# Kernel tuning notes

Measured on AMD Instinct MI355X. Metric: run time of the kernel, lower is better.

The kernel has to match this reference:

```python
import jax, jax.numpy as jnp
import numpy as np

NUM_NODES = 5000
NUM_RELS = 100
MAX_VISIT = 20
EMB = 128
HID = 128
OUT = 25
LAYERS = 3
B = 32
N_TOTAL = 100000
E_TOTAL = 400000
DECAY_RATE = 0.01
EPS = 0.0  # GIN-style self-loop weight (self_attn=0.0, not trained)


def setup_inputs() -> dict:
    key = jax.random.key(0)
    ks = jax.random.split(key, 24)
    f32 = jnp.float32
    # graph structure
    node_ids = jax.random.randint(ks[0], (N_TOTAL,), 0, NUM_NODES)
    rel_ids = jax.random.randint(ks[1], (E_TOTAL,), 0, NUM_RELS)
    edge_index = jax.random.randint(ks[2], (2, E_TOTAL), 0, N_TOTAL)
    batch = jnp.sort(jax.random.randint(ks[3], (N_TOTAL,), 0, B))
    # binary visit/ehr indicators (float, fed into Linear layers / masks)
    visit_node = (jax.random.uniform(ks[4], (B, MAX_VISIT, NUM_NODES)) < 0.05).astype(f32)
    ehr_nodes = (jax.random.uniform(ks[5], (B, NUM_NODES)) < 0.2).astype(f32)
    # embedding tables + projection
    node_table = jax.random.normal(ks[6], (NUM_NODES, EMB), f32) * 0.02
    rel_table = jax.random.normal(ks[7], (NUM_RELS, EMB), f32) * 0.02
    lin_w = jax.random.normal(ks[8], (HID, EMB), f32) * (1.0 / np.sqrt(EMB))
    lin_b = jnp.zeros((HID,), f32)
    # per-layer params, stacked on leading axis
    alpha_w = jax.random.normal(ks[9], (LAYERS, NUM_NODES, NUM_NODES), f32) * np.sqrt(1.0 / NUM_NODES)
    alpha_b = jnp.zeros((LAYERS, NUM_NODES), f32)
    beta_w = jax.random.normal(ks[10], (LAYERS, 1, NUM_NODES), f32) * np.sqrt(2.0 / (NUM_NODES + 1))
    beta_b = jnp.zeros((LAYERS, 1), f32)
    wr_w = jax.random.normal(ks[11], (LAYERS, 1, HID), f32) * (1.0 / np.sqrt(HID))
    wr_b = jnp.zeros((LAYERS, 1), f32)
    conv_w = jax.random.normal(ks[12], (LAYERS, HID, HID), f32) * (1.0 / np.sqrt(HID))
    conv_b = jnp.zeros((LAYERS, HID), f32)
    # final MLP (joint mode: Linear(2H,H) -> ReLU -> Linear(H,OUT))
    mlp_w1 = jax.random.normal(ks[13], (HID, 2 * HID), f32) * (1.0 / np.sqrt(2 * HID))
    mlp_b1 = jnp.zeros((HID,), f32)
    mlp_w2 = jax.random.normal(ks[14], (OUT, HID), f32) * (1.0 / np.sqrt(HID))
    mlp_b2 = jnp.zeros((OUT,), f32)
    return dict(node_table=node_table, rel_table=rel_table, lin_w=lin_w, lin_b=lin_b,
                alpha_w=alpha_w, alpha_b=alpha_b, beta_w=beta_w, beta_b=beta_b,
                wr_w=wr_w, wr_b=wr_b, conv_w=conv_w, conv_b=conv_b,
                mlp_w1=mlp_w1, mlp_b1=mlp_b1, mlp_w2=mlp_w2, mlp_b2=mlp_b2,
                visit_node=visit_node, ehr_nodes=ehr_nodes,
                node_ids=node_ids, rel_ids=rel_ids, edge_index=edge_index, batch=batch)


def reference(node_table, rel_table, lin_w, lin_b, alpha_w, alpha_b, beta_w, beta_b,
              wr_w, wr_b, conv_w, conv_b, mlp_w1, mlp_b1, mlp_w2, mlp_b2,
              visit_node, ehr_nodes, node_ids, rel_ids, edge_index, batch):
    # embed + project (lin is shared by nodes and relations)
    x = node_table[node_ids] @ lin_w.T + lin_b        # [N, H]
    e = rel_table[rel_ids] @ lin_w.T + lin_b          # [E, H]
    src, dst = edge_index[0], edge_index[1]
    N = x.shape[0]
    # temporal decay lambda_j = exp(gamma * (V - j)), shape [1, V, 1]
    j = jnp.arange(MAX_VISIT, dtype=x.dtype)
    lam = jnp.exp(DECAY_RATE * (MAX_VISIT - j))[None, :, None]
    for l in range(LAYERS):
        # alpha: softmax over visit dim of Linear(num_nodes -> num_nodes)
        alpha = jax.nn.softmax(jnp.einsum('bvn,mn->bvm', visit_node, alpha_w[l]) + alpha_b[l], axis=1)  # [B,V,num_nodes]
        # beta: tanh(Linear(num_nodes -> 1)) * lambda_j
        beta = jnp.tanh(jnp.einsum('bvn,on->bvo', visit_node, beta_w[l]) + beta_b[l]) * lam  # [B,V,1]
        attn = jnp.sum(alpha * beta, axis=1)          # [B, num_nodes]
        # per-edge attention gathered at the source node j of each edge
        attn_e = attn[batch[src], node_ids[src]][:, None]   # [E,1]
        # BAT message: relu(x_j * attn_j + W_R(e) * e), scatter-add at dst
        w_rel = e @ wr_w[l].T + wr_b[l]               # [E,1]
        msg = jax.nn.relu(x[src] * attn_e + w_rel * e)
        agg = jax.ops.segment_sum(msg, dst, num_segments=N)
        x = (agg + (1.0 + EPS) * x) @ conv_w[l].T + conv_b[l]
    # patient_mode='joint': global mean pool + masked EHR-node mean
    cnt = jax.ops.segment_sum(jnp.ones((N,), x.dtype), batch, num_segments=B)
    x_graph = jax.ops.segment_sum(x, batch, num_segments=B) / jnp.maximum(cnt, 1.0)[:, None]
    mask = ehr_nodes[batch, node_ids]                 # [N], 0/1
    mcnt = jax.ops.segment_sum(mask, batch, num_segments=B)
    x_node = jax.ops.segment_sum(x * mask[:, None], batch, num_segments=B) / jnp.maximum(mcnt, 1.0)[:, None]
    h = jnp.concatenate([x_graph, x_node], axis=1)    # [B, 2H]
    h = jax.nn.relu(h @ mlp_w1.T + mlp_b1)
    return h @ mlp_w2.T + mlp_b2                      # [B, OUT] logits


if __name__ == '__main__':
    out = reference(**setup_inputs())
    print(out.shape)
```

## Files before the change

### kernel.cpp

```cpp
#include <hip/hip_runtime.h>
#include <stdint.h>

#define NNODE 5000
#define NREL  100
#define MAXV  20
#define NH    128
#define NBATCH 32
#define NTOT  100000
#define ETOT  400000
#define AKP   5056

typedef float  f32x4  __attribute__((ext_vector_type(4)));
typedef __bf16 bf16x8 __attribute__((ext_vector_type(8)));

static __device__ __forceinline__ f32x4 f4zero(){ f32x4 z; z[0]=0.f; z[1]=0.f; z[2]=0.f; z[3]=0.f; return z; }
static __device__ __forceinline__ int swz(int row, int byte_in_row){ return byte_in_row ^ ((row & 7) << 4); }

__global__ __launch_bounds__(256) void gemm128f(
    const float* __restrict__ A0, const float* __restrict__ A1, int boundary, int M,
    const float* __restrict__ W, const float* __restrict__ bias,
    float* __restrict__ D0, float* __restrict__ D1)
{
  __shared__ __bf16 As[64*128];
  __shared__ __bf16 Bh[128*128];
  __shared__ __bf16 Bl[128*128];
  char* AsB = (char*)As; char* BhB = (char*)Bh; char* BlB = (char*)Bl;
  const int tid = threadIdx.x, lane = tid & 63, w = tid >> 6;
  const int r0 = blockIdx.x * 64;
  {
    const int row = tid >> 2, c0 = (tid & 3) * 32;
    const int gr = r0 + row;
    bf16x8 t8[4];
    if (gr < M){
      const float* src = (gr < boundary) ? (A0 + (size_t)gr * NH) : (A1 + (size_t)(gr - boundary) * NH);
      const f32x4* gp = (const f32x4*)(src + c0);
      #pragma unroll
      for (int j = 0; j < 8; ++j){
        f32x4 v = gp[j];
        #pragma unroll
        for (int q = 0; q < 4; ++q) t8[j>>1][(j&1)*4+q] = (__bf16)v[q];
      }
    } else {
      #pragma unroll
      for (int j = 0; j < 4; ++j)
        #pragma unroll
        for (int q = 0; q < 8; ++q) t8[j][q] = (__bf16)0.0f;
    }
    #pragma unroll
    for (int j = 0; j < 4; ++j) *(bf16x8*)(AsB + swz(row, row*256 + c0*2 + j*16) ) = t8[j];
  }
  {
    const int row = tid >> 1, c0 = (tid & 1) * 64;
    bf16x8 th[8], tl[8];
    const f32x4* gp = (const f32x4*)(W + row*NH + c0);
    #pragma unroll
    for (int j = 0; j < 16; ++j){
      f32x4 v = gp[j];
      #pragma unroll
      for (int q = 0; q < 4; ++q){
        float f = v[q];
        __bf16 h = (__bf16)f;
        th[j>>1][(j&1)*4+q] = h;
        tl[j>>1][(j&1)*4+q] = (__bf16)(f - (float)h);
      }
    }
    #pragma unroll
    for (int j = 0; j < 8; ++j){
      *(bf16x8*)(BhB + swz(row, row*256 + c0*2 + j*16)) = th[j];
      *(bf16x8*)(BlB + swz(row, row*256 + c0*2 + j*16)) = tl[j];
    }
  }
  __syncthreads();
  f32x4 acc[8];
  #pragma unroll
  for (int n = 0; n < 8; ++n) acc[n] = f4zero();
  #pragma unroll
  for (int kk = 0; kk < 4; ++kk){
    const int kb = kk*64 + (lane>>4)*16;
    const int arow = w*16 + (lane&15);
    bf16x8 af = *(const bf16x8*)(AsB + swz(arow, arow*256 + kb));
    #pragma unroll
    for (int nj = 0; nj < 8; ++nj){
      const int brow = nj*16 + (lane&15);
      bf16x8 bh = *(const bf16x8*)(BhB + swz(brow, brow*256 + kb));
      acc[nj] = __builtin_amdgcn_mfma_f32_16x16x32_bf16(af, bh, acc[nj], 0, 0, 0);
      bf16x8 bl = *(const bf16x8*)(BlB + swz(brow, brow*256 + kb));
      acc[nj] = __builtin_amdgcn_mfma_f32_16x16x32_bf16(af, bl, acc[nj], 0, 0, 0);
    }
  }
  const int rb = r0 + w*16 + ((lane>>4)*4);
  #pragma unroll
  for (int q = 0; q < 4; ++q){
    const int row = rb + q;
    if (row < M){
      #pragma unroll
      for (int nj = 0; nj < 8; ++nj){
        const int col = nj*16 + (lane&15);
        float* dp = (row < boundary) ? (D0 + (size_t)row*NH + col) : (D1 + (size_t)(row-boundary)*NH + col);
        *dp = acc[nj][q] + bias[col];
      }
    }
  }
}

__global__ __launch_bounds__(256) void alpha_gemm(
    const float* __restrict__ W, const __bf16* __restrict__ VNb, float* __restrict__ S)
{
  __shared__ __bf16 As[64*64];
  __shared__ __bf16 Bs[64*64];
  char* AsB = (char*)As; char* BsB = (char*)Bs;
  const int tid = threadIdx.x, lane = tid & 63, w = tid >> 6;
  const int bid = blockIdx.x;
  const int xcd = bid & 7, idx = bid >> 3;
  const int logical = (xcd < 6 ? xcd*99 : 6*99 + (xcd-6)*98) + idx;
  const int mt = logical / 10, bt = logical % 10;

  const int srow = tid >> 2, sc = tid & 3;
  const int gm = mt*64 + srow;
  const bool m_ok = (gm < NNODE);
  const float* wrow = W + (size_t)gm * NNODE;
  const __bf16* vrow = VNb + (size_t)(bt*64 + srow) * AKP;

  f32x4 acc[4];
  #pragma unroll
  for (int n = 0; n < 4; ++n) acc[n] = f4zero();

  bf16x8 avr[2];
  f32x4  bvr[4];
  #pragma unroll
  for (int h = 0; h < 2; ++h) avr[h] = *(const bf16x8*)(vrow + sc*16 + h*8);
  if (m_ok){
    const f32x4* gp = (const f32x4*)(wrow + sc*16);
    #pragma unroll
    for (int j = 0; j < 4; ++j) bvr[j] = gp[j];
  } else {
    #pragma unroll
    for (int j = 0; j < 4; ++j) bvr[j] = f4zero();
  }

  for (int kt = 0; kt < 79; ++kt){
    __syncthreads();
    #pragma unroll
    for (int h = 0; h < 2; ++h)
      *(bf16x8*)(AsB + swz(srow, srow*128 + sc*32 + h*16)) = avr[h];
    {
      bf16x8 t8[2];
      #pragma unroll
      for (int j = 0; j < 4; ++j)
        #pragma unroll
        for (int q = 0; q < 4; ++q) t8[j>>1][(j&1)*4+q] = (__bf16)bvr[j][q];
      #pragma unroll
      for (int h = 0; h < 2; ++h)
        *(bf16x8*)(BsB + swz(srow, srow*128 + sc*32 + h*16)) = t8[h];
    }
    __syncthreads();
    if (kt < 78){
      const int k0 = (kt+1)*64;
      #pragma unroll
      for (int h = 0; h < 2; ++h) avr[h] = *(const bf16x8*)(vrow + k0 + sc*16 + h*8);
      if (!m_ok){
        #pragma unroll
        for (int j = 0; j < 4; ++j) bvr[j] = f4zero();
      } else if (kt + 1 < 78){
        const f32x4* gp = (const f32x4*)(wrow + k0 + sc*16);
        #pragma unroll
        for (int j = 0; j < 4; ++j) bvr[j] = gp[j];
      } else {
        #pragma unroll
        for (int j = 0; j < 4; ++j){
          f32x4 v;
          #pragma unroll
          for (int q = 0; q < 4; ++q){
            int c = k0 + sc*16 + j*4 + q;
            v[q] = (c < NNODE) ? wrow[c] : 0.f;
          }
          bvr[j] = v;
        }
      }
    }
    #pragma unroll
    for (int kk = 0; kk < 2; ++kk){
      const int kb = kk*64 + (lane>>4)*16;
      const int arow = w*16 + (lane&15);
      bf16x8 af = *(const bf16x8*)(AsB + swz(arow, arow*128 + kb));
      #pragma unroll
      for (int nj = 0; nj < 4; ++nj){
        const int brow = nj*16 + (lane&15);
        bf16x8 bf = *(const bf16x8*)(BsB + swz(brow, brow*128 + kb));
        acc[nj] = __builtin_amdgcn_mfma_f32_16x16x32_bf16(af, bf, acc[nj], 0, 0, 0);
      }
    }
  }
  const int rb = bt*64 + w*16 + ((lane>>4)*4);
  #pragma unroll
  for (int nj = 0; nj < 4; ++nj){
    const int col = mt*64 + nj*16 + (lane&15);
    if (col < NNODE){
      #pragma unroll
      for (int q = 0; q < 4; ++q)
        S[(size_t)(rb + q)*NNODE + col] = acc[nj][q];
    }
  }
}

__global__ __launch_bounds__(256) void vn_kernel(const float* __restrict__ visit, __bf16* __restrict__ VNb){
  int id = blockIdx.x*256 + threadIdx.x;
  if (id >= 640*632) return;
  int r = id / 632, c8 = (id % 632) * 8;
  bf16x8 o;
  #pragma unroll
  for (int j = 0; j < 8; ++j){
    int c = c8 + j;
    float v = (c < NNODE) ? visit[(size_t)r*NNODE + c] : 0.f;
    o[j] = (__bf16)v;
  }
  *(bf16x8*)(VNb + (size_t)r*AKP + c8) = o;
}

__global__ __launch_bounds__(256) void x_init_kernel(const float* __restrict__ nproj, const int* __restrict__ nids, float* __restrict__ x){
  int id = blockIdx.x*256 + threadIdx.x;
  int r = id >> 7, f = id & 127;
  x[id] = nproj[(size_t)nids[r]*NH + f];
}

__global__ __launch_bounds__(256) void edge_pre_kernel(const int* __restrict__ esrc, const int* __restrict__ batch, const int* __restrict__ nids, int* __restrict__ eix){
  int e = blockIdx.x*256 + threadIdx.x;
  if (e >= ETOT) return;
  int s = esrc[e];
  eix[e] = batch[s]*NNODE + nids[s];
}

__global__ __launch_bounds__(256) void hist_kernel(const int* __restrict__ edst, int* __restrict__ cnt){
  int e = blockIdx.x*256 + threadIdx.x;
  if (e >= ETOT) return;
  atomicAdd(&cnt[edst[e]], 1);
}

__global__ __launch_bounds__(256) void scan1_kernel(const int* __restrict__ cnt, int* __restrict__ offp, int* __restrict__ bsum){
  __shared__ int sh[256];
  int t = threadIdx.x;
  int base = blockIdx.x*1024 + t*4;
  int v[4]; int ts = 0;
  #pragma unroll
  for (int i = 0; i < 4; ++i){ v[i] = (base+i < NTOT) ? cnt[base+i] : 0; ts += v[i]; }
  sh[t] = ts; __syncthreads();
  for (int o = 1; o < 256; o <<= 1){
    int xv = 0; if (t >= o) xv = sh[t-o];
    __syncthreads();
    if (t >= o) sh[t] += xv;
    __syncthreads();
  }
  int run = sh[t] - ts;
  #pragma unroll
  for (int i = 0; i < 4; ++i){ if (base+i < NTOT) offp[base+i] = run; run += v[i]; }
  if (t == 255) bsum[blockIdx.x] = sh[255];
}

__global__ __launch_bounds__(128) void scan2_kernel(const int* __restrict__ bsum, int* __restrict__ bpre){
  __shared__ int sh[128];
  int t = threadIdx.x;
  int v = (t < 98) ? bsum[t] : 0;
  sh[t] = v; __syncthreads();
  for (int o = 1; o < 128; o <<= 1){
    int xv = 0; if (t >= o) xv = sh[t-o];
    __syncthreads();
    if (t >= o) sh[t] += xv;
    __syncthreads();
  }
  if (t < 98) bpre[t] = sh[t] - v;
}

__global__ __launch_bounds__(256) void scan3_kernel(const int* __restrict__ bpre, int* __restrict__ offp, int* __restrict__ curp){
  int i = blockIdx.x*256 + threadIdx.x;
  if (i >= NTOT) return;
  int v = offp[i] + bpre[i >> 10];
  offp[i] = v; curp[i] = v;
}

__global__ __launch_bounds__(256) void scatter_kernel(const int* __restrict__ edst, int* __restrict__ curp, int* __restrict__ perm){
  int e = blockIdx.x*256 + threadIdx.x;
  if (e >= ETOT) return;
  int p = atomicAdd(&curp[edst[e]], 1);
  perm[p] = e;
}

__global__ __launch_bounds__(256) void beta_kernel(const float* __restrict__ visit, const float* __restrict__ bw, const float* __restrict__ bb, float* __restrict__ beta){
  int wid = blockIdx.x*4 + (threadIdx.x >> 6);
  int lane = threadIdx.x & 63;
  if (wid >= 3*640) return;
  int l = wid / 640, r = wid % 640, vv = r % MAXV;
  const float* vp = visit + (size_t)r*NNODE;
  const float* wp = bw + (size_t)l*NNODE;
  float acc = 0.f;
  for (int n = lane; n < NNODE; n += 64) acc += vp[n]*wp[n];
  #pragma unroll
  for (int o = 32; o > 0; o >>= 1) acc += __shfl_down(acc, o);
  if (lane == 0) beta[wid] = tanhf(acc + bb[l]) * expf(0.01f*(float)(MAXV - vv));
}

__global__ __launch_bounds__(320) void wrel_kernel(const float* __restrict__ relp, const float* __restrict__ wrw, const float* __restrict__ wrb, float* __restrict__ wrel){
  int t = threadIdx.x;
  if (t >= 300) return;
  int l = t / 100, r = t % 100;
  float acc = 0.f;
  for (int h = 0; h < NH; ++h) acc += relp[r*NH + h]*wrw[l*NH + h];
  wrel[t] = acc + wrb[l];
}

__global__ __launch_bounds__(256) void attn_kernel(const float* __restrict__ S, const float* __restrict__ beta_l, float* __restrict__ attn){
  int id = blockIdx.x*256 + threadIdx.x;
  if (id >= NBATCH*NNODE) return;
  int b = id / NNODE;
  const float* sp = S + (size_t)(b*MAXV)*NNODE + (id % NNODE);
  float mx = -1e30f;
  #pragma unroll
  for (int v = 0; v < MAXV; ++v) mx = fmaxf(mx, sp[(size_t)v*NNODE]);
  float den = 0.f, num = 0.f;
  #pragma unroll
  for (int v = 0; v < MAXV; ++v){
    float e = expf(sp[(size_t)v*NNODE] - mx);
    den += e; num += e * beta_l[b*MAXV + v];
  }
  attn[id] = num / den;
}

__global__ __launch_bounds__(256) void agg_kernel(
    const float* __restrict__ x, const float* __restrict__ attn,
    const float* __restrict__ relp, const float* __restrict__ wrel_l,
    const int* __restrict__ eix, const int* __restrict__ esrc, const int* __restrict__ erel,
    const int* __restrict__ offp, const int* __restrict__ cnt, const int* __restrict__ perm,
    float* __restrict__ y)
{
  int node = blockIdx.x*4 + (threadIdx.x >> 6);
  int lane = threadIdx.x & 63;
  float a1 = x[(size_t)node*NH + lane];
  float a2 = x[(size_t)node*NH + 64 + lane];
  int st = offp[node], n = cnt[node];
  for (int t = 0; t < n; ++t){
    int eid = perm[st + t];
    int s  = esrc[eid];
    int rr = erel[eid];
    float at = attn[eix[eid]];
    float wv = wrel_l[rr];
    float x1 = x[(size_t)s*NH + lane];
    float x2 = x[(size_t)s*NH + 64 + lane];
    float r1 = relp[rr*NH + lane];
    float r2 = relp[rr*NH + 64 + lane];
    a1 += fmaxf(x1*at + wv*r1, 0.f);
    a2 += fmaxf(x2*at + wv*r2, 0.f);
  }
  y[(size_t)node*NH + lane] = a1;
  y[(size_t)node*NH + 64 + lane] = a2;
}

__global__ __launch_bounds__(128) void pool_kernel(
    const float* __restrict__ x, const int* __restrict__ batch, const int* __restrict__ nids, const float* __restrict__ ehr,
    float* __restrict__ sum_g, float* __restrict__ sum_n, float* __restrict__ cntb, float* __restrict__ mcntb)
{
  int t = threadIdx.x;
  int r0 = blockIdx.x*128;
  int rend = (r0 + 128 < NTOT) ? r0 + 128 : NTOT;
  float ag = 0.f, an = 0.f, c = 0.f, mc = 0.f; int cur = -1;
  for (int r = r0; r < rend; ++r){
    int b = batch[r];
    if (b != cur){
      if (cur >= 0){
        atomicAdd(&sum_g[cur*NH + t], ag);
        atomicAdd(&sum_n[cur*NH + t], an);
        if (t == 0){ atomicAdd(&cntb[cur], c); atomicAdd(&mcntb[cur], mc); }
      }
      cur = b; ag = an = c = mc = 0.f;
    }
    float xv = x[(size_t)r*NH + t];
    float m = ehr[b*NNODE + nids[r]];
    ag += xv; an += m*xv; c += 1.f; mc += m;
  }
  if (cur >= 0){
    atomicAdd(&sum_g[cur*NH + t], ag);
    atomicAdd(&sum_n[cur*NH + t], an);
    if (t == 0){ atomicAdd(&cntb[cur], c); atomicAdd(&mcntb[cur], mc); }
  }
}

__global__ __launch_bounds__(256) void mlp_kernel(
    const float* __restrict__ sum_g, const float* __restrict__ sum_n, const float* __restrict__ cntb, const float* __restrict__ mcntb,
    const float* __restrict__ w1, const float* __restrict__ b1, const float* __restrict__ w2, const float* __restrict__ b2,
    float* __restrict__ out)
{
  __shared__ float hs[8*256];
  __shared__ float w1s[64*132];
  __shared__ float hid[8*128];
  int t = threadIdx.x;
  int b0 = blockIdx.x * 8;
  for (int e = t; e < 8*256; e += 256){
    int bb = e >> 8, c = e & 255;
    int gb = b0 + bb;
    float v;
    if (c < NH) v = sum_g[gb*NH + c] / fmaxf(cntb[gb], 1.f);
    else        v = sum_n[gb*NH + (c-NH)] / fmaxf(mcntb[gb], 1.f);
    hs[e] = v;
  }
  __syncthreads();
  float acc4[4] = {0.f,0.f,0.f,0.f};
  int j = t & 127, half = t >> 7;
  for (int c = 0; c < 4; ++c){
    for (int e = t; e < 8192; e += 256){
      int jj = e >> 6, kk = e & 63;
      w1s[kk*132 + jj] = w1[jj*256 + c*64 + kk];
    }
    __syncthreads();
    #pragma unroll
    for (int p = 0; p < 4; ++p){
      int bb = p*2 + half;
      float a = 0.f;
      for (int k = 0; k < 64; ++k) a += hs[bb*256 + c*64 + k] * w1s[k*132 + j];
      acc4[p] += a;
    }
    __syncthreads();
  }
  #pragma unroll
  for (int p = 0; p < 4; ++p){
    int bb = p*2 + half;
    hid[bb*128 + j] = fmaxf(acc4[p] + b1[j], 0.f);
  }
  __syncthreads();
  if (t < 8*25){
    int bb = t / 25, o = t % 25;
    float a = b2[o];
    for (int k = 0; k < NH; ++k) a += hid[bb*128 + k] * w2[o*NH + k];
    out[(size_t)(b0 + bb)*25 + o] = a;
  }
}

extern "C" void kernel_launch(void* const* d_in, const int* in_sizes, int n_in,
                              void* d_out, int out_size, void* d_ws, size_t ws_size,
                              hipStream_t stream)
{
  const float* node_table = (const float*)d_in[0];
  const float* rel_table  = (const float*)d_in[1];
  const float* lin_w  = (const float*)d_in[2];
  const float* lin_b  = (const float*)d_in[3];
  const float* alpha_w = (const float*)d_in[4];
  const float* beta_w = (const float*)d_in[6];
  const float* beta_b = (const float*)d_in[7];
  const float* wr_w   = (const float*)d_in[8];
  const float* wr_b   = (const float*)d_in[9];
  const float* conv_w = (const float*)d_in[10];
  const float* conv_b = (const float*)d_in[11];
  const float* mlp_w1 = (const float*)d_in[12];
  const float* mlp_b1 = (const float*)d_in[13];
  const float* mlp_w2 = (const float*)d_in[14];
  const float* mlp_b2 = (const float*)d_in[15];
  const float* visit  = (const float*)d_in[16];
  const float* ehr    = (const float*)d_in[17];
  const int* nids     = (const int*)d_in[18];
  const int* rel_ids  = (const int*)d_in[19];
  const int* eindex   = (const int*)d_in[20];
  const int* batch    = (const int*)d_in[21];
  const int* esrc = eindex;
  const int* edst = eindex + ETOT;

  char* wsb = (char*)d_ws;
  size_t off = 0;
  auto alloc = [&](size_t bytes) -> void* {
    void* p = wsb + off;
    off += (bytes + 255) & ~(size_t)255;
    return p;
  };
  float*  x     = (float*)alloc((size_t)NTOT*NH*4);
  float*  y     = (float*)alloc((size_t)NTOT*NH*4);
  float*  S     = (float*)alloc((size_t)640*NNODE*4);
  __bf16* VNb   = (__bf16*)alloc((size_t)640*AKP*2);
  float*  nproj = (float*)alloc((size_t)NNODE*NH*4);
  float*  rproj = (float*)alloc((size_t)NREL*NH*4);
  float*  attn  = (float*)alloc((size_t)NBATCH*NNODE*4);
  float*  beta  = (float*)alloc(3*640*4);
  float*  wrel  = (float*)alloc(3*100*4);
  int*    eix   = (int*)alloc((size_t)ETOT*4);
  int*    cnt   = (int*)alloc((size_t)NTOT*4);
  int*    offp  = (int*)alloc((size_t)NTOT*4);
  int*    curp  = (int*)alloc((size_t)NTOT*4);
  int*    perm  = (int*)alloc((size_t)ETOT*4);
  int*    bsum  = (int*)alloc(512);
  int*    bpre  = (int*)alloc(512);
  float*  pool  = (float*)alloc((size_t)(NBATCH*NH*2 + 64)*4);
  float*  sum_g = pool;
  float*  sum_n = pool + NBATCH*NH;
  float*  cntb  = pool + NBATCH*NH*2;
  float*  mcntb = cntb + NBATCH;

  hipMemsetAsync(cnt, 0, (size_t)NTOT*4, stream);
  hipMemsetAsync(pool, 0, (size_t)(NBATCH*NH*2 + 64)*4, stream);

  gemm128f<<<80, 256, 0, stream>>>(node_table, rel_table, NNODE, NNODE+NREL, lin_w, lin_b, nproj, rproj);
  x_init_kernel<<<50000, 256, 0, stream>>>(nproj, nids, x);
  vn_kernel<<<1580, 256, 0, stream>>>(visit, VNb);
  edge_pre_kernel<<<1563, 256, 0, stream>>>(esrc, batch, nids, eix);
  hist_kernel<<<1563, 256, 0, stream>>>(edst, cnt);
  scan1_kernel<<<98, 256, 0, stream>>>(cnt, offp, bsum);
  scan2_kernel<<<1, 128, 0, stream>>>(bsum, bpre);
  scan3_kernel<<<391, 256, 0, stream>>>(bpre, offp, curp);
  scatter_kernel<<<1563, 256, 0, stream>>>(edst, curp, perm);
  beta_kernel<<<480, 256, 0, stream>>>(visit, beta_w, beta_b, beta);
  wrel_kernel<<<1, 320, 0, stream>>>(rproj, wr_w, wr_b, wrel);

  for (int l = 0; l < 3; ++l){
    alpha_gemm<<<790, 256, 0, stream>>>(alpha_w + (size_t)l*NNODE*NNODE, VNb, S);
    attn_kernel<<<625, 256, 0, stream>>>(S, beta + l*640, attn);
    agg_kernel<<<25000, 256, 0, stream>>>(x, attn, rproj, wrel + l*100, eix, esrc, rel_ids, offp, cnt, perm, y);
    gemm128f<<<1563, 256, 0, stream>>>(y, y, NTOT, NTOT, conv_w + (size_t)l*NH*NH, conv_b + (size_t)l*NH, x, x);
  }
  pool_kernel<<<782, 128, 0, stream>>>(x, batch, nids, ehr, sum_g, sum_n, cntb, mcntb);
  mlp_kernel<<<4, 256, 0, stream>>>(sum_g, sum_n, cntb, mcntb, mlp_w1, mlp_b1, mlp_w2, mlp_b2, (float*)d_out);
}
```

Measured before the change: 1.367 ms.

## Pre-split weights, pack CSR edge records, double K-tile and rows per GEMM block

Four separate changes. Weight hi/lo bf16 splitting moves to a one-time wsplit kernel, and gemm128f now processes two 64-row tiles per block so the staged weights are reused. The alpha GEMM K-tile grows from 64 to 128 (AKP padded to 5120), halving the loop iterations and barriers. The scatter now writes packed int4 edge records (src, rel, eix) in CSR order, so aggregation does one 16-byte load per edge instead of a chain of dependent indirect loads. The costs are more registers and LDS in alpha_gemm, which may cut occupancy, and a larger edge array.

```diff
diff --git a/kernel.cpp b/kernel.cpp
--- a/kernel.cpp
+++ b/kernel.cpp
@@ -8,17 +8,37 @@
 #define NBATCH 32
 #define NTOT  100000
 #define ETOT  400000
-#define AKP   5056
+#define AKP   5120
 
 typedef float  f32x4  __attribute__((ext_vector_type(4)));
 typedef __bf16 bf16x8 __attribute__((ext_vector_type(8)));
+typedef __bf16 bf16x4 __attribute__((ext_vector_type(4)));
 
 static __device__ __forceinline__ f32x4 f4zero(){ f32x4 z; z[0]=0.f; z[1]=0.f; z[2]=0.f; z[3]=0.f; return z; }
 static __device__ __forceinline__ int swz(int row, int byte_in_row){ return byte_in_row ^ ((row & 7) << 4); }
 
+__global__ __launch_bounds__(256) void wsplit_kernel(
+    const float* __restrict__ lin_w, const float* __restrict__ conv_w, __bf16* __restrict__ Whl)
+{
+  int id = blockIdx.x*256 + threadIdx.x;
+  int mat = id >> 12, elem4 = (id & 4095) * 4;
+  const float* src = (mat == 0) ? (lin_w + elem4) : (conv_w + (size_t)(mat-1)*16384 + elem4);
+  f32x4 v = *(const f32x4*)src;
+  bf16x4 h4, l4;
+  #pragma unroll
+  for (int q = 0; q < 4; ++q){
+    float f = v[q];
+    __bf16 h = (__bf16)f;
+    h4[q] = h; l4[q] = (__bf16)(f - (float)h);
+  }
+  __bf16* dst = Whl + (size_t)mat*2*16384;
+  *(bf16x4*)(dst + elem4) = h4;
+  *(bf16x4*)(dst + 16384 + elem4) = l4;
+}
+
 __global__ __launch_bounds__(256) void gemm128f(
     const float* __restrict__ A0, const float* __restrict__ A1, int boundary, int M,
-    const float* __restrict__ W, const float* __restrict__ bias,
+    const __bf16* __restrict__ Whl, const float* __restrict__ bias,
     float* __restrict__ D0, float* __restrict__ D1)
 {
   __shared__ __bf16 As[64*128];
@@ -26,78 +46,73 @@
   __shared__ __bf16 Bl[128*128];
   char* AsB = (char*)As; char* BhB = (char*)Bh; char* BlB = (char*)Bl;
   const int tid = threadIdx.x, lane = tid & 63, w = tid >> 6;
-  const int r0 = blockIdx.x * 64;
   {
-    const int row = tid >> 2, c0 = (tid & 3) * 32;
-    const int gr = r0 + row;
-    bf16x8 t8[4];
-    if (gr < M){
-      const float* src = (gr < boundary) ? (A0 + (size_t)gr * NH) : (A1 + (size_t)(gr - boundary) * NH);
-      const f32x4* gp = (const f32x4*)(src + c0);
-      #pragma unroll
-      for (int j = 0; j < 8; ++j){
-        f32x4 v = gp[j];
-        #pragma unroll
-        for (int q = 0; q < 4; ++q) t8[j>>1][(j&1)*4+q] = (__bf16)v[q];
+    const int row = tid >> 1, half = tid & 1;
+    const __bf16* sh = Whl + row*128 + half*64;
+    const __bf16* sl = sh + 16384;
+    #pragma unroll
+    for (int j = 0; j < 8; ++j){
+      bf16x8 vh = *(const bf16x8*)(sh + j*8);
+      bf16x8 vl = *(const bf16x8*)(sl + j*8);
+      *(bf16x8*)(BhB + swz(row, row*256 + half*128 + j*16)) = vh;
+      *(bf16x8*)(BlB + swz(row, row*256 + half*128 + j*16)) = vl;
+    }
+  }
+  #pragma unroll
+  for (int t = 0; t < 2; ++t){
+    const int r0 = blockIdx.x*128 + t*64;
+    if (t == 1) __syncthreads();
+    {
+      const int row = tid >> 2, c0 = (tid & 3) * 32;
+      const int gr = r0 + row;
+      bf16x8 t8[4];
+      if (gr < M){
+        const float* src = (gr < boundary) ? (A0 + (size_t)gr * NH) : (A1 + (size_t)(gr - boundary) * NH);
+        const f32x4* gp = (const f32x4*)(src + c0);
+        #pragma unroll
+        for (int j = 0; j < 8; ++j){
+          f32x4 v = gp[j];
+          #pragma unroll
+          for (int q = 0; q < 4; ++q) t8[j>>1][(j&1)*4+q] = (__bf16)v[q];
+        }
+      } else {
+        #pragma unroll
+        for (int j = 0; j < 4; ++j)
+          #pragma unroll
+          for (int q = 0; q < 8; ++q) t8[j][q] = (__bf16)0.0f;
       }
-    } else {
-      #pragma unroll
-      for (int j = 0; j < 4; ++j)
-        #pragma unroll
-        for (int q = 0; q < 8; ++q) t8[j][q] = (__bf16)0.0f;
-    }
-    #pragma unroll
-    for (int j = 0; j < 4; ++j) *(bf16x8*)(AsB + swz(row, row*256 + c0*2 + j*16) ) = t8[j];
-  }
-  {
-    const int row = tid >> 1, c0 = (tid & 1) * 64;
-    bf16x8 th[8], tl[8];
-    const f32x4* gp = (const f32x4*)(W + row*NH + c0);
-    #pragma unroll
-    for (int j = 0; j < 16; ++j){
-      f32x4 v = gp[j];
-      #pragma unroll
-      for (int q = 0; q < 4; ++q){
-        float f = v[q];
-        __bf16 h = (__bf16)f;
-        th[j>>1][(j&1)*4+q] = h;
-        tl[j>>1][(j&1)*4+q] = (__bf16)(f - (float)h);
+      #pragma unroll
+      for (int j = 0; j < 4; ++j) *(bf16x8*)(AsB + swz(row, row*256 + c0*2 + j*16)) = t8[j];
+    }
+    __syncthreads();
+    f32x4 acc[8];
+    #pragma unroll
+    for (int n = 0; n < 8; ++n) acc[n] = f4zero();
+    #pragma unroll
+    for (int kk = 0; kk < 4; ++kk){
+      const int kb = kk*64 + (lane>>4)*16;
+      const int arow = w*16 + (lane&15);
+      bf16x8 af = *(const bf16x8*)(AsB + swz(arow, arow*256 + kb));
+      #pragma unroll
+      for (int nj = 0; nj < 8; ++nj){
+        const int brow = nj*16 + (lane&15);
+        bf16x8 bh = *(const bf16x8*)(BhB + swz(brow, brow*256 + kb));
+        acc[nj] = __builtin_amdgcn_mfma_f32_16x16x32_bf16(af, bh, acc[nj], 0, 0, 0);
+        bf16x8 bl = *(const bf16x8*)(BlB + swz(brow, brow*256 + kb));
+        acc[nj] = __builtin_amdgcn_mfma_f32_16x16x32_bf16(af, bl, acc[nj], 0, 0, 0);
       }
     }
-    #pragma unroll
-    for (int j = 0; j < 8; ++j){
-      *(bf16x8*)(BhB + swz(row, row*256 + c0*2 + j*16)) = th[j];
-      *(bf16x8*)(BlB + swz(row, row*256 + c0*2 + j*16)) = tl[j];
-    }
-  }
-  __syncthreads();
-  f32x4 acc[8];
-  #pragma unroll
-  for (int n = 0; n < 8; ++n) acc[n] = f4zero();
-  #pragma unroll
-  for (int kk = 0; kk < 4; ++kk){
-    const int kb = kk*64 + (lane>>4)*16;
-    const int arow = w*16 + (lane&15);
-    bf16x8 af = *(const bf16x8*)(AsB + swz(arow, arow*256 + kb));
-    #pragma unroll
-    for (int nj = 0; nj < 8; ++nj){
-      const int brow = nj*16 + (lane&15);
-      bf16x8 bh = *(const bf16x8*)(BhB + swz(brow, brow*256 + kb));
-      acc[nj] = __builtin_amdgcn_mfma_f32_16x16x32_bf16(af, bh, acc[nj], 0, 0, 0);
-      bf16x8 bl = *(const bf16x8*)(BlB + swz(brow, brow*256 + kb));
-      acc[nj] = __builtin_amdgcn_mfma_f32_16x16x32_bf16(af, bl, acc[nj], 0, 0, 0);
-    }
-  }
-  const int rb = r0 + w*16 + ((lane>>4)*4);
-  #pragma unroll
-  for (int q = 0; q < 4; ++q){
-    const int row = rb + q;
-    if (row < M){
-      #pragma unroll
-      for (int nj = 0; nj < 8; ++nj){
-        const int col = nj*16 + (lane&15);
-        float* dp = (row < boundary) ? (D0 + (size_t)row*NH + col) : (D1 + (size_t)(row-boundary)*NH + col);
-        *dp = acc[nj][q] + bias[col];
+    const int rb = r0 + w*16 + ((lane>>4)*4);
+    #pragma unroll
+    for (int q = 0; q < 4; ++q){
+      const int row = rb + q;
+      if (row < M){
+        #pragma unroll
+        for (int nj = 0; nj < 8; ++nj){
+          const int col = nj*16 + (lane&15);
+          float* dp = (row < boundary) ? (D0 + (size_t)row*NH + col) : (D1 + (size_t)(row-boundary)*NH + col);
+          *dp = acc[nj][q] + bias[col];
+        }
       }
     }
   }
@@ -106,8 +121,8 @@
 __global__ __launch_bounds__(256) void alpha_gemm(
     const float* __restrict__ W, const __bf16* __restrict__ VNb, float* __restrict__ S)
 {
-  __shared__ __bf16 As[64*64];
-  __shared__ __bf16 Bs[64*64];
+  __shared__ __bf16 As[64*128];
+  __shared__ __bf16 Bs[64*128];
   char* AsB = (char*)As; char* BsB = (char*)Bs;
   const int tid = threadIdx.x, lane = tid & 63, w = tid >> 6;
   const int bid = blockIdx.x;
@@ -125,53 +140,53 @@
   #pragma unroll
   for (int n = 0; n < 4; ++n) acc[n] = f4zero();
 
-  bf16x8 avr[2];
-  f32x4  bvr[4];
-  #pragma unroll
-  for (int h = 0; h < 2; ++h) avr[h] = *(const bf16x8*)(vrow + sc*16 + h*8);
+  bf16x8 avr[4];
+  f32x4  bvr[8];
+  #pragma unroll
+  for (int h = 0; h < 4; ++h) avr[h] = *(const bf16x8*)(vrow + sc*32 + h*8);
   if (m_ok){
-    const f32x4* gp = (const f32x4*)(wrow + sc*16);
-    #pragma unroll
-    for (int j = 0; j < 4; ++j) bvr[j] = gp[j];
+    const f32x4* gp = (const f32x4*)(wrow + sc*32);
+    #pragma unroll
+    for (int j = 0; j < 8; ++j) bvr[j] = gp[j];
   } else {
     #pragma unroll
-    for (int j = 0; j < 4; ++j) bvr[j] = f4zero();
-  }
-
-  for (int kt = 0; kt < 79; ++kt){
-    __syncthreads();
-    #pragma unroll
-    for (int h = 0; h < 2; ++h)
-      *(bf16x8*)(AsB + swz(srow, srow*128 + sc*32 + h*16)) = avr[h];
+    for (int j = 0; j < 8; ++j) bvr[j] = f4zero();
+  }
+
+  for (int kt = 0; kt < 40; ++kt){
+    __syncthreads();
+    #pragma unroll
+    for (int h = 0; h < 4; ++h)
+      *(bf16x8*)(AsB + swz(srow, srow*256 + sc*64 + h*16)) = avr[h];
     {
-      bf16x8 t8[2];
-      #pragma unroll
-      for (int j = 0; j < 4; ++j)
+      bf16x8 t8[4];
+      #pragma unroll
+      for (int j = 0; j < 8; ++j)
         #pragma unroll
         for (int q = 0; q < 4; ++q) t8[j>>1][(j&1)*4+q] = (__bf16)bvr[j][q];
       #pragma unroll
-      for (int h = 0; h < 2; ++h)
-        *(bf16x8*)(BsB + swz(srow, srow*128 + sc*32 + h*16)) = t8[h];
-    }
-    __syncthreads();
-    if (kt < 78){
-      const int k0 = (kt+1)*64;
-      #pragma unroll
-      for (int h = 0; h < 2; ++h) avr[h] = *(const bf16x8*)(vrow + k0 + sc*16 + h*8);
+      for (int h = 0; h < 4; ++h)
+        *(bf16x8*)(BsB + swz(srow, srow*256 + sc*64 + h*16)) = t8[h];
+    }
+    __syncthreads();
+    if (kt < 39){
+      const int k0 = (kt+1)*128;
+      #pragma unroll
+      for (int h = 0; h < 4; ++h) avr[h] = *(const bf16x8*)(vrow + k0 + sc*32 + h*8);
       if (!m_ok){
         #pragma unroll
-        for (int j = 0; j < 4; ++j) bvr[j] = f4zero();
-      } else if (kt + 1 < 78){
-        const f32x4* gp = (const f32x4*)(wrow + k0 + sc*16);
-        #pragma unroll
-        for (int j = 0; j < 4; ++j) bvr[j] = gp[j];
+        for (int j = 0; j < 8; ++j) bvr[j] = f4zero();
+      } else if (kt + 1 < 39){
+        const f32x4* gp = (const f32x4*)(wrow + k0 + sc*32);
+        #pragma unroll
+        for (int j = 0; j < 8; ++j) bvr[j] = gp[j];
       } else {
         #pragma unroll
-        for (int j = 0; j < 4; ++j){
+        for (int j = 0; j < 8; ++j){
           f32x4 v;
           #pragma unroll
           for (int q = 0; q < 4; ++q){
-            int c = k0 + sc*16 + j*4 + q;
+            int c = k0 + sc*32 + j*4 + q;
             v[q] = (c < NNODE) ? wrow[c] : 0.f;
           }
           bvr[j] = v;
@@ -179,14 +194,14 @@
       }
     }
     #pragma unroll
-    for (int kk = 0; kk < 2; ++kk){
+    for (int kk = 0; kk < 4; ++kk){
       const int kb = kk*64 + (lane>>4)*16;
       const int arow = w*16 + (lane&15);
-      bf16x8 af = *(const bf16x8*)(AsB + swz(arow, arow*128 + kb));
+      bf16x8 af = *(const bf16x8*)(AsB + swz(arow, arow*256 + kb));
       #pragma unroll
       for (int nj = 0; nj < 4; ++nj){
         const int brow = nj*16 + (lane&15);
-        bf16x8 bf = *(const bf16x8*)(BsB + swz(brow, brow*128 + kb));
+        bf16x8 bf = *(const bf16x8*)(BsB + swz(brow, brow*256 + kb));
         acc[nj] = __builtin_amdgcn_mfma_f32_16x16x32_bf16(af, bf, acc[nj], 0, 0, 0);
       }
     }
@@ -205,8 +220,8 @@
 
 __global__ __launch_bounds__(256) void vn_kernel(const float* __restrict__ visit, __bf16* __restrict__ VNb){
   int id = blockIdx.x*256 + threadIdx.x;
-  if (id >= 640*632) return;
-  int r = id / 632, c8 = (id % 632) * 8;
+  if (id >= 640*640) return;
+  int r = id / 640, c8 = (id % 640) * 8;
   bf16x8 o;
   #pragma unroll
   for (int j = 0; j < 8; ++j){
@@ -277,11 +292,15 @@
   offp[i] = v; curp[i] = v;
 }
 
-__global__ __launch_bounds__(256) void scatter_kernel(const int* __restrict__ edst, int* __restrict__ curp, int* __restrict__ perm){
+__global__ __launch_bounds__(256) void scatter_kernel(
+    const int* __restrict__ edst, const int* __restrict__ esrc, const int* __restrict__ erel,
+    const int* __restrict__ eix, int* __restrict__ curp, int4* __restrict__ epack)
+{
   int e = blockIdx.x*256 + threadIdx.x;
   if (e >= ETOT) return;
   int p = atomicAdd(&curp[edst[e]], 1);
-  perm[p] = e;
+  int4 pk; pk.x = esrc[e]; pk.y = erel[e]; pk.z = eix[e]; pk.w = 0;
+  epack[p] = pk;
 }
 
 __global__ __launch_bounds__(256) void beta_kernel(const float* __restrict__ visit, const float* __restrict__ bw, const float* __restrict__ bb, float* __restrict__ beta){
@@ -327,8 +346,8 @@
 __global__ __launch_bounds__(256) void agg_kernel(
     const float* __restrict__ x, const float* __restrict__ attn,
     const float* __restrict__ relp, const float* __restrict__ wrel_l,
-    const int* __restrict__ eix, const int* __restrict__ esrc, const int* __restrict__ erel,
-    const int* __restrict__ offp, const int* __restrict__ cnt, const int* __restrict__ perm,
+    const int4* __restrict__ epack,
+    const int* __restrict__ offp, const int* __restrict__ cnt,
     float* __restrict__ y)
 {
   int node = blockIdx.x*4 + (threadIdx.x >> 6);
@@ -336,18 +355,15 @@
   float a1 = x[(size_t)node*NH + lane];
   float a2 = x[(size_t)node*NH + 64 + lane];
   int st = offp[node], n = cnt[node];
+  const int4* ep = epack + st;
   for (int t = 0; t < n; ++t){
-    int eid = perm[st + t];
-    int s  = esrc[eid];
-    int rr = erel[eid];
-    float at = attn[eix[eid]];
-    float wv = wrel_l[rr];
-    float x1 = x[(size_t)s*NH + lane];
-    float x2 = x[(size_t)s*NH + 64 + lane];
-    float r1 = relp[rr*NH + lane];
-    float r2 = relp[rr*NH + 64 + lane];
-    a1 += fmaxf(x1*at + wv*r1, 0.f);
-    a2 += fmaxf(x2*at + wv*r2, 0.f);
+    int4 pk = ep[t];
+    float at = attn[pk.z];
+    float wv = wrel_l[pk.y];
+    const float* xs = x + (size_t)pk.x*NH;
+    const float* rp = relp + pk.y*NH;
+    a1 += fmaxf(xs[lane]      * at + wv * rp[lane],      0.f);
+    a2 += fmaxf(xs[64 + lane] * at + wv * rp[64 + lane], 0.f);
   }
   y[(size_t)node*NH + lane] = a1;
   y[(size_t)node*NH + 64 + lane] = a2;
@@ -471,6 +487,7 @@
   float*  y     = (float*)alloc((size_t)NTOT*NH*4);
   float*  S     = (float*)alloc((size_t)640*NNODE*4);
   __bf16* VNb   = (__bf16*)alloc((size_t)640*AKP*2);
+  __bf16* Whl   = (__bf16*)alloc((size_t)4*2*16384*2);
   float*  nproj = (float*)alloc((size_t)NNODE*NH*4);
   float*  rproj = (float*)alloc((size_t)NREL*NH*4);
   float*  attn  = (float*)alloc((size_t)NBATCH*NNODE*4);
@@ -480,7 +497,7 @@
   int*    cnt   = (int*)alloc((size_t)NTOT*4);
   int*    offp  = (int*)alloc((size_t)NTOT*4);
   int*    curp  = (int*)alloc((size_t)NTOT*4);
-  int*    perm  = (int*)alloc((size_t)ETOT*4);
+  int4*   epack = (int4*)alloc((size_t)ETOT*16);
   int*    bsum  = (int*)alloc(512);
   int*    bpre  = (int*)alloc(512);
   float*  pool  = (float*)alloc((size_t)(NBATCH*NH*2 + 64)*4);
@@ -492,23 +509,24 @@
   hipMemsetAsync(cnt, 0, (size_t)NTOT*4, stream);
   hipMemsetAsync(pool, 0, (size_t)(NBATCH*NH*2 + 64)*4, stream);
 
-  gemm128f<<<80, 256, 0, stream>>>(node_table, rel_table, NNODE, NNODE+NREL, lin_w, lin_b, nproj, rproj);
+  wsplit_kernel<<<64, 256, 0, stream>>>(lin_w, conv_w, Whl);
+  gemm128f<<<40, 256, 0, stream>>>(node_table, rel_table, NNODE, NNODE+NREL, Whl, lin_b, nproj, rproj);
   x_init_kernel<<<50000, 256, 0, stream>>>(nproj, nids, x);
-  vn_kernel<<<1580, 256, 0, stream>>>(visit, VNb);
+  vn_kernel<<<1600, 256, 0, stream>>>(visit, VNb);
   edge_pre_kernel<<<1563, 256, 0, stream>>>(esrc, batch, nids, eix);
   hist_kernel<<<1563, 256, 0, stream>>>(edst, cnt);
   scan1_kernel<<<98, 256, 0, stream>>>(cnt, offp, bsum);
   scan2_kernel<<<1, 128, 0, stream>>>(bsum, bpre);
   scan3_kernel<<<391, 256, 0, stream>>>(bpre, offp, curp);
-  scatter_kernel<<<1563, 256, 0, stream>>>(edst, curp, perm);
+  scatter_kernel<<<1563, 256, 0, stream>>>(edst, esrc, rel_ids, eix, curp, epack);
   beta_kernel<<<480, 256, 0, stream>>>(visit, beta_w, beta_b, beta);
   wrel_kernel<<<1, 320, 0, stream>>>(rproj, wr_w, wr_b, wrel);
 
   for (int l = 0; l < 3; ++l){
     alpha_gemm<<<790, 256, 0, stream>>>(alpha_w + (size_t)l*NNODE*NNODE, VNb, S);
     attn_kernel<<<625, 256, 0, stream>>>(S, beta + l*640, attn);
-    agg_kernel<<<25000, 256, 0, stream>>>(x, attn, rproj, wrel + l*100, eix, esrc, rel_ids, offp, cnt, perm, y);
-    gemm128f<<<1563, 256, 0, stream>>>(y, y, NTOT, NTOT, conv_w + (size_t)l*NH*NH, conv_b + (size_t)l*NH, x, x);
+    agg_kernel<<<25000, 256, 0, stream>>>(x, attn, rproj, wrel + l*100, epack, offp, cnt, y);
+    gemm128f<<<782, 256, 0, stream>>>(y, y, NTOT, NTOT, Whl + (size_t)(1+l)*2*16384, conv_b + (size_t)l*NH, x, x);
   }
   pool_kernel<<<782, 128, 0, stream>>>(x, batch, nids, ehr, sum_g, sum_n, cntb, mcntb);
   mlp_kernel<<<4, 256, 0, stream>>>(sum_g, sum_n, cntb, mcntb, mlp_w1, mlp_b1, mlp_w2, mlp_b2, (float*)d_out);
```

Measured after the change: 1.479 ms. +8.2%, slower.
